# Performance work log

Measured on AMD Instinct MI355X. Metric: run time of the kernel, lower is better.

The kernel has to match this reference:

```python
import jax, jax.numpy as jnp
import numpy as np

D = 1024      # d_model
H = 16        # n_heads
KVH = 4       # num_kv_heads
DH = D // H   # head_dim = 64
CHUNK = 256
SDIM = 128
MG = 8        # m_global
B, T = 4, 4096


def setup_inputs() -> dict:
    key = jax.random.key(0)
    ks = jax.random.split(key, 12)
    s = 0.02
    mk = lambda i, shape: jax.random.normal(ks[i], shape, jnp.float32) * s
    return dict(
        x=jax.random.normal(ks[0], (B, T, D), jnp.float32),
        state=jnp.zeros((B, SDIM), jnp.float32),
        Wq=mk(1, (D, D)), Wk=mk(2, (KVH * DH, D)), Wv=mk(3, (KVH * DH, D)),
        Wo=mk(4, (D, D)), bo=jnp.zeros((D,), jnp.float32),
        ln_attn_g=jnp.ones((D,), jnp.float32), ln_attn_b=jnp.zeros((D,), jnp.float32),
        ln_ffn_g=jnp.ones((D,), jnp.float32), ln_ffn_b=jnp.zeros((D,), jnp.float32),
        W1=mk(5, (4 * D, D)), b1=jnp.zeros((4 * D,), jnp.float32),
        W2=mk(6, (D, 4 * D)), b2=jnp.zeros((D,), jnp.float32),
        Wsp=mk(7, (SDIM, D)), bsp=jnp.zeros((SDIM,), jnp.float32),
        Wsi=mk(8, (D, SDIM)), bsi=jnp.zeros((D,), jnp.float32),
        gtok=mk(9, (MG, D)),
    )


def _ln(x, g, b):
    m = x.mean(-1, keepdims=True)
    v = ((x - m) ** 2).mean(-1, keepdims=True)
    return (x - m) / jnp.sqrt(v + 1e-5) * g + b


def reference(x, state, Wq, Wk, Wv, Wo, bo, ln_attn_g, ln_attn_b,
              ln_ffn_g, ln_ffn_b, W1, b1, W2, b2, Wsp, bsp, Wsi, bsi, gtok):
    Bn, Tn, Dn = x.shape
    nchunks = Tn // CHUNK
    Tc = MG + CHUNK            # tokens per attention call (globals + chunk)
    G = H // KVH               # query heads per KV head
    causal = jnp.tril(jnp.ones((Tc, Tc), bool))
    scale = 1.0 / np.sqrt(DH).astype(np.float32)

    def step(st, chunk):  # st:[B,SDIM], chunk:[B,CHUNK,D]
        h = _ln(chunk, ln_attn_g, ln_attn_b) + (st @ Wsi.T + bsi)[:, None, :]
        h_in = jnp.concatenate([jnp.broadcast_to(gtok, (Bn, MG, Dn)), h], axis=1)
        q = (h_in @ Wq.T).reshape(Bn, Tc, H, DH)
        k = (h_in @ Wk.T).reshape(Bn, Tc, KVH, DH)
        v = (h_in @ Wv.T).reshape(Bn, Tc, KVH, DH)
        # GQA: group query heads over shared KV heads
        qg = q.reshape(Bn, Tc, KVH, G, DH)
        scores = jnp.einsum('bqhgd,bkhd->bhgqk', qg * scale, k)
        scores = jnp.where(causal, scores, -jnp.inf)
        attn = jax.nn.softmax(scores, axis=-1)
        o = jnp.einsum('bhgqk,bkhd->bqhgd', attn, v).reshape(Bn, Tc, Dn)
        y = (o @ Wo.T + bo)[:, MG:, :]
        c = chunk + y
        ff = jax.nn.gelu(_ln(c, ln_ffn_g, ln_ffn_b) @ W1.T + b1, approximate=False) @ W2.T + b2
        c = c + ff
        new_st = c.mean(axis=1) @ Wsp.T + bsp
        return new_st, c

    chunks = x.reshape(Bn, nchunks, CHUNK, Dn).transpose(1, 0, 2, 3)
    final_state, outs = jax.lax.scan(step, state, chunks)
    y_full = outs.transpose(1, 0, 2, 3).reshape(Bn, Tn, Dn)
    return y_full, final_state
```

## Files before the change

kernel.cpp:

```cpp
#include <hip/hip_runtime.h>
#include <hip/hip_bf16.h>

#define Dm    1024
#define Hn    16
#define KVH   4
#define DH    64
#define CHUNK 256
#define SDIM  128
#define MG    8
#define Bn    4
#define Tn    4096
#define TC    264
#define NSTEP 16
#define TD    4194304L

typedef __attribute__((ext_vector_type(8))) short short8;
typedef __attribute__((ext_vector_type(4))) float floatx4;
typedef __hip_bfloat16 bf16;

__device__ __forceinline__ void gl16(const void* g, void* l) {
    using GP = const __attribute__((address_space(1))) char*;
    using LP = __attribute__((address_space(3))) char*;
    __builtin_amdgcn_global_load_lds((GP)g, (LP)l, 16, 0, 0);
}
__device__ __forceinline__ float b2f(short s) {
    unsigned int u = ((unsigned int)(unsigned short)s) << 16;
    float f; __builtin_memcpy(&f, &u, 4); return f;
}
__device__ __forceinline__ short f2b(float f) {
    bf16 h = __float2bfloat16(f);
    short s; __builtin_memcpy(&s, &h, 2); return s;
}


__global__ __launch_bounds__(512) void vcopy_k(const float* __restrict__ s, float* __restrict__ d, int n) {
    int i = blockIdx.x * 512 + threadIdx.x;
    if (i < n) d[i] = s[i];
}

__global__ __launch_bounds__(256) void cvt_bf16_k(const float* __restrict__ s, bf16* __restrict__ d, int n4) {
    int i = blockIdx.x * 256 + threadIdx.x;
    if (i >= n4) return;
    float4 v = ((const float4*)s)[i];
    bf16* o = d + i * 4;
    o[0] = __float2bfloat16(v.x); o[1] = __float2bfloat16(v.y);
    o[2] = __float2bfloat16(v.z); o[3] = __float2bfloat16(v.w);
}

__global__ __launch_bounds__(256) void wsiT_k(const float* __restrict__ Wsi, bf16* __restrict__ WsiT) {
    int idx = blockIdx.x * 256 + threadIdx.x;
    int s = idx >> 10, d = idx & 1023;
    WsiT[idx] = __float2bfloat16(Wsi[d * SDIM + s]);
}

__global__ __launch_bounds__(64) void bfused_k(const bf16* __restrict__ wqkv, const float* __restrict__ bsi,
                                               float* __restrict__ bfused) {
    int n = blockIdx.x * 64 + threadIdx.x;
    const bf16* wr = wqkv + (long)n * 1024;
    float a = 0.f;
    for (int k8 = 0; k8 < 128; ++k8) {
        short8 wv = *(const short8*)(wr + k8 * 8);
#pragma unroll
        for (int e = 0; e < 8; ++e) a += b2f(wv[e]) * bsi[k8 * 8 + e];
    }
    bfused[n] = a;
}

__global__ __launch_bounds__(64) void sib_k(const float* __restrict__ st, const bf16* __restrict__ Wf,
                                            const float* __restrict__ bfused, float* __restrict__ sib) {
    int b = blockIdx.x, n = blockIdx.y * 64 + threadIdx.x;
    const float* sr = st + b * SDIM;
    const bf16* wr = Wf + (long)n * SDIM;
    float a = bfused[n];
#pragma unroll
    for (int k8 = 0; k8 < 16; ++k8) {
        short8 wv = *(const short8*)(wr + k8 * 8);
#pragma unroll
        for (int e = 0; e < 8; ++e) a += sr[k8 * 8 + e] * b2f(wv[e]);
    }
    sib[b * 1536 + n] = a;
}

__global__ __launch_bounds__(192) void addsi_k(bf16* __restrict__ qkv_s, const float* __restrict__ sib) {
    int b = blockIdx.x, r = MG + blockIdx.y, n0 = threadIdx.x * 8;
    bf16* p = qkv_s + ((long)(b * TC + r) * 1536 + n0);
    const float* sb = sib + b * 1536 + n0;
    short8 v = *(const short8*)p;
    short8 o;
#pragma unroll
    for (int e = 0; e < 8; ++e) o[e] = f2b(b2f(v[e]) + sb[e]);
    *(short8*)p = o;
}

__global__ __launch_bounds__(256) void lng_k(const float* __restrict__ x, const float* __restrict__ gtok,
                                             const float* __restrict__ g, const float* __restrict__ be,
                                             bf16* __restrict__ lnxg, int gstep) {
    int bx = blockIdx.x, b = blockIdx.y, tid = threadIdx.x;
    int sl = bx / 264, r = bx - sl * 264;
    bf16* orow = lnxg + (long)((sl * 4 + b) * 264 + r) * 1024 + tid * 4;
    if (r < MG) {
        float4 v = *(const float4*)(gtok + r * 1024 + tid * 4);
        orow[0] = __float2bfloat16(v.x); orow[1] = __float2bfloat16(v.y);
        orow[2] = __float2bfloat16(v.z); orow[3] = __float2bfloat16(v.w);
        return;
    }
    const float* row = x + (long)b * TD + ((long)(gstep * 4 + sl) * 256 + (r - MG)) * 1024;
    float4 v = *(const float4*)(row + tid * 4);
    float s = v.x + v.y + v.z + v.w;
    float q = v.x * v.x + v.y * v.y + v.z * v.z + v.w * v.w;
    for (int off = 32; off > 0; off >>= 1) { s += __shfl_down(s, off); q += __shfl_down(q, off); }
    __shared__ float red[10];
    int w = tid >> 6;
    if ((tid & 63) == 0) { red[w] = s; red[4 + w] = q; }
    __syncthreads();
    if (tid == 0) {
        float ts = red[0] + red[1] + red[2] + red[3];
        float tq = red[4] + red[5] + red[6] + red[7];
        float mean = ts * (1.f / Dm);
        float var = tq * (1.f / Dm) - mean * mean;
        red[8] = mean;
        red[9] = rsqrtf(var + 1e-5f);
    }
    __syncthreads();
    float mean = red[8], rstd = red[9];
    int d = tid * 4;
    float4 gv = *(const float4*)(g + d);
    float4 bv = *(const float4*)(be + d);
    orow[0] = __float2bfloat16((v.x - mean) * rstd * gv.x + bv.x);
    orow[1] = __float2bfloat16((v.y - mean) * rstd * gv.y + bv.y);
    orow[2] = __float2bfloat16((v.z - mean) * rstd * gv.z + bv.z);
    orow[3] = __float2bfloat16((v.w - mean) * rstd * gv.w + bv.w);
}

template<int BN>
__global__ __launch_bounds__(256) void gemm64(
    const bf16* __restrict__ A, const bf16* __restrict__ W,
    int M, int N, int K, int kspan,
    bf16* __restrict__ Cb, int ldc, const float* __restrict__ bias, int gelu,
    float* __restrict__ Cpart, long partMN)
{
    constexpr int NSEG = 4 + BN / 16;
    constexpr int SEGW = NSEG / 4;
    constexpr int FC   = BN / 64;
    constexpr int WN   = BN / 4;
    constexpr int HALFB = NSEG * 1024;
    constexpr int PHB   = 2 * HALFB;
    __shared__ short S[PHB];

    int tid = threadIdx.x;
    int w = tid >> 6, l = tid & 63;
    int m0 = blockIdx.y << 6, n0 = blockIdx.x * BN;
    long kb = (long)blockIdx.z * kspan;

    const bf16* gp[SEGW];
    int so[SEGW];
#pragma unroll
    for (int si = 0; si < SEGW; ++si) {
        int s = w + si * 4;
        const bf16* base = (s < 4) ? (A + (long)(m0 + s * 16 + (l >> 2)) * K)
                                   : (W + (long)(n0 + (s - 4) * 16 + (l >> 2)) * K);
        gp[si] = base + ((l & 3) << 3) + kb;
        so[si] = s * 1024 + l * 16;
    }
    char* cS = (char*)S;

    floatx4 acc[4][FC];
#pragma unroll
    for (int t = 0; t < 4; ++t)
#pragma unroll
        for (int u = 0; u < FC; ++u) acc[t][u] = (floatx4){0.f, 0.f, 0.f, 0.f};

    int arow = l & 15;
    int acol = (l >> 4) << 3;
    int np = kspan >> 6;

#define STAGE(p)                                                         \
    {                                                                    \
        int kt_ = (p) << 6;                                              \
        char* b_ = cS + ((p) & 1) * PHB;                                 \
        _Pragma("unroll")                                                \
        for (int si = 0; si < SEGW; ++si) {                              \
            gl16(gp[si] + kt_, b_ + so[si]);                             \
            gl16(gp[si] + kt_ + 32, b_ + HALFB + so[si]);                \
        }                                                                \
    }

    STAGE(0)
    for (int p = 0; p < np; ++p) {
        if (p + 1 < np) {
            STAGE(p + 1)
            if constexpr (SEGW == 2) asm volatile("s_waitcnt vmcnt(4)" ::: "memory");
            else                     asm volatile("s_waitcnt vmcnt(6)" ::: "memory");
        } else {
            asm volatile("s_waitcnt vmcnt(0)" ::: "memory");
        }
        __builtin_amdgcn_s_barrier();
        __builtin_amdgcn_sched_barrier(0);
        const short* buf = S + (p & 1) * (PHB / 2);
#pragma unroll
        for (int kh = 0; kh < 2; ++kh) {
            const short* hb = buf + kh * (HALFB / 2);
            short8 a[4], b[FC];
#pragma unroll
            for (int t = 0; t < 4; ++t)
                a[t] = *(const short8*)&hb[(t * 16 + arow) * 32 + acol];
#pragma unroll
            for (int u = 0; u < FC; ++u)
                b[u] = *(const short8*)&hb[2048 + (w * WN + u * 16 + arow) * 32 + acol];
#pragma unroll
            for (int t = 0; t < 4; ++t)
#pragma unroll
                for (int u = 0; u < FC; ++u)
                    acc[t][u] = __builtin_amdgcn_mfma_f32_16x16x32_bf16(a[t], b[u], acc[t][u], 0, 0, 0);
        }
        __builtin_amdgcn_sched_barrier(0);
        __builtin_amdgcn_s_barrier();
    }
#undef STAGE

    int crow0 = m0 + ((l >> 4) << 2);
    int ccol0 = n0 + w * WN + (l & 15);
    if (Cpart) {
        float* pp = Cpart + (long)blockIdx.z * partMN;
#pragma unroll
        for (int t = 0; t < 4; ++t)
#pragma unroll
            for (int rr = 0; rr < 4; ++rr) {
                int m = crow0 + t * 16 + rr;
                if (m >= M) continue;
#pragma unroll
                for (int u = 0; u < FC; ++u)
                    pp[(long)m * N + ccol0 + u * 16] = acc[t][u][rr];
            }
    } else {
#pragma unroll
        for (int t = 0; t < 4; ++t)
#pragma unroll
            for (int rr = 0; rr < 4; ++rr) {
                int m = crow0 + t * 16 + rr;
                if (m >= M) continue;
                bf16* crow = Cb + (long)m * ldc;
#pragma unroll
                for (int u = 0; u < FC; ++u) {
                    int n = ccol0 + u * 16;
                    float v = acc[t][u][rr];
                    if (bias) v += bias[n];
                    if (gelu) v = 0.5f * v * (1.f + erff(v * 0.70710678118654752f));
                    crow[n] = __float2bfloat16(v);
                }
            }
    }
}

__global__ __launch_bounds__(256) void reduce_ln_k(const float* __restrict__ part,
                                                   const float* __restrict__ bo,
                                                   const float* __restrict__ x,
                                                   float* __restrict__ out, long roff,
                                                   const float* __restrict__ g,
                                                   const float* __restrict__ be,
                                                   bf16* __restrict__ t_ln) {
    int m = blockIdx.x;
    int b = m >> 8, r = m & 255;
    int tid = threadIdx.x;
    long ro = (long)b * TD + (roff + r) * 1024L + tid * 4;
    int pi = m * 256 + tid;
    float4 s  = ((const float4*)part)[pi];
    float4 p2 = ((const float4*)(part + 1048576))[pi];
    float4 bv = ((const float4*)bo)[tid];
    float4 rv = *(const float4*)(x + ro);
    float c0 = s.x + p2.x + bv.x + rv.x;
    float c1 = s.y + p2.y + bv.y + rv.y;
    float c2 = s.z + p2.z + bv.z + rv.z;
    float c3 = s.w + p2.w + bv.w + rv.w;
    *(float4*)(out + ro) = make_float4(c0, c1, c2, c3);
    float sum = c0 + c1 + c2 + c3;
    float sq  = c0 * c0 + c1 * c1 + c2 * c2 + c3 * c3;
    for (int off = 32; off > 0; off >>= 1) { sum += __shfl_down(sum, off); sq += __shfl_down(sq, off); }
    __shared__ float red[10];
    int w = tid >> 6;
    if ((tid & 63) == 0) { red[w] = sum; red[4 + w] = sq; }
    __syncthreads();
    if (tid == 0) {
        float ts = red[0] + red[1] + red[2] + red[3];
        float tq = red[4] + red[5] + red[6] + red[7];
        float mean = ts * (1.f / Dm);
        float var = tq * (1.f / Dm) - mean * mean;
        red[8] = mean;
        red[9] = rsqrtf(var + 1e-5f);
    }
    __syncthreads();
    float mean = red[8], rstd = red[9];
    float4 gv = ((const float4*)g)[tid];
    float4 bev = ((const float4*)be)[tid];
    bf16* orow = t_ln + (long)(b * CHUNK + r) * Dm + tid * 4;
    orow[0] = __float2bfloat16((c0 - mean) * rstd * gv.x + bev.x);
    orow[1] = __float2bfloat16((c1 - mean) * rstd * gv.y + bev.y);
    orow[2] = __float2bfloat16((c2 - mean) * rstd * gv.z + bev.z);
    orow[3] = __float2bfloat16((c3 - mean) * rstd * gv.w + bev.w);
}

__global__ __launch_bounds__(256) void reduce_colpart_k(const float* __restrict__ part,
                                                        const float* __restrict__ bias,
                                                        float* __restrict__ out, long roff,
                                                        float* __restrict__ colp) {
    int b = blockIdx.x, rg = blockIdx.y, tid = threadIdx.x;
    float4 bv = ((const float4*)bias)[tid];
    float4 cs = make_float4(0.f, 0.f, 0.f, 0.f);
#pragma unroll
    for (int r8 = 0; r8 < 8; ++r8) {
        int r = rg * 8 + r8;
        int pi = (b * 256 + r) * 256 + tid;
        float4 s  = ((const float4*)part)[pi];
        float4 p2 = ((const float4*)(part + 1048576))[pi];
        long ro = (long)b * TD + (roff + r) * 1024L + tid * 4;
        float4 rv = *(const float4*)(out + ro);
        float4 v = make_float4(s.x + p2.x + bv.x + rv.x, s.y + p2.y + bv.y + rv.y,
                               s.z + p2.z + bv.z + rv.z, s.w + p2.w + bv.w + rv.w);
        *(float4*)(out + ro) = v;
        cs.x += v.x; cs.y += v.y; cs.z += v.z; cs.w += v.w;
    }
    *(float4*)(colp + ((b * 32 + rg) << 10) + tid * 4) = cs;
}

__global__ __launch_bounds__(256) void attn_mfma_k(const bf16* __restrict__ qkv, bf16* __restrict__ o_mat) {
    int qc = blockIdx.x, head = blockIdx.y, b = blockIdx.z;
    int kvh = head >> 2;
    int tid = threadIdx.x, w = tid >> 6, l = tid & 63;
    int m16 = l & 15, h4 = l >> 4;

    __shared__ short Qs[64][64];
    __shared__ short Ks[64][64];
    __shared__ short Vt[64][64];
    __shared__ short Ps[4][16][64];

    const long rowq0 = (long)b * TC + MG + qc * 64;
    const bf16* kbase = qkv + ((long)b * TC) * 1536 + 1024 + kvh * DH;
    const bf16* vbase = kbase + 256;

#pragma unroll
    for (int p = 0; p < 2; ++p) {
        int rr = p * 32 + (tid >> 3);
        gl16(qkv + (rowq0 + rr) * 1536 + head * DH + (tid & 7) * 8, &Qs[rr][(tid & 7) * 8]);
    }

    float a_m[4] = {-1e30f, -1e30f, -1e30f, -1e30f};
    float a_l[4] = {0.f, 0.f, 0.f, 0.f};
    floatx4 acc_o[4];
#pragma unroll
    for (int dt = 0; dt < 4; ++dt) acc_o[dt] = (floatx4){0.f, 0.f, 0.f, 0.f};
    short8 aq[2];

    int qtok0 = MG + qc * 64 + w * 16 + h4 * 4;
    int ntiles = qc + 2;

    for (int t = 0; t < ntiles; ++t) {
        int jt = t * 64;
#pragma unroll
        for (int p = 0; p < 2; ++p) {
            int rr = p * 32 + (tid >> 3);
            int gk = min(jt + rr, TC - 1);
            gl16(kbase + (long)gk * 1536 + (tid & 7) * 8, &Ks[rr][(tid & 7) * 8]);
        }
#pragma unroll
        for (int p = 0; p < 2; ++p) {
            int cg = p * 4 + w;
            int gk = min(jt + l, TC - 1);
            short8 vv = *(const short8*)(vbase + (long)gk * 1536 + cg * 8);
#pragma unroll
            for (int e = 0; e < 8; ++e) Vt[cg * 8 + e][l] = vv[e];
        }
        __syncthreads();
        if (t == 0) {
            aq[0] = *(const short8*)&Qs[w * 16 + m16][h4 * 8];
            aq[1] = *(const short8*)&Qs[w * 16 + m16][32 + h4 * 8];
        }
        floatx4 s[4];
#pragma unroll
        for (int st = 0; st < 4; ++st) {
            s[st] = (floatx4){0.f, 0.f, 0.f, 0.f};
#pragma unroll
            for (int c = 0; c < 2; ++c) {
                short8 kf = *(const short8*)&Ks[st * 16 + m16][c * 32 + h4 * 8];
                s[st] = __builtin_amdgcn_mfma_f32_16x16x32_bf16(aq[c], kf, s[st], 0, 0, 0);
            }
        }
#pragma unroll
        for (int st = 0; st < 4; ++st) {
            int keyg = jt + st * 16 + m16;
#pragma unroll
            for (int r = 0; r < 4; ++r) {
                float v = s[st][r] * 0.125f;
                s[st][r] = (keyg > qtok0 + r) ? -1e30f : v;
            }
        }
#pragma unroll
        for (int r = 0; r < 4; ++r) {
            float tm = fmaxf(fmaxf(s[0][r], s[1][r]), fmaxf(s[2][r], s[3][r]));
            tm = fmaxf(tm, __shfl_xor(tm, 1));
            tm = fmaxf(tm, __shfl_xor(tm, 2));
            tm = fmaxf(tm, __shfl_xor(tm, 4));
            tm = fmaxf(tm, __shfl_xor(tm, 8));
            float mn = fmaxf(a_m[r], tm);
            float rs = __expf(a_m[r] - mn);
            a_m[r] = mn;
            float ps = 0.f;
#pragma unroll
            for (int st = 0; st < 4; ++st) {
                float p = __expf(s[st][r] - mn);
                s[st][r] = p;
                ps += p;
            }
            ps += __shfl_xor(ps, 1); ps += __shfl_xor(ps, 2);
            ps += __shfl_xor(ps, 4); ps += __shfl_xor(ps, 8);
            a_l[r] = a_l[r] * rs + ps;
#pragma unroll
            for (int dt = 0; dt < 4; ++dt) acc_o[dt][r] *= rs;
#pragma unroll
            for (int st = 0; st < 4; ++st) {
                Ps[w][h4 * 4 + r][st * 16 + m16] = f2b(s[st][r]);
            }
        }
#pragma unroll
        for (int c = 0; c < 2; ++c) {
            short8 ap = *(const short8*)&Ps[w][m16][c * 32 + h4 * 8];
#pragma unroll
            for (int dt = 0; dt < 4; ++dt) {
                short8 vf = *(const short8*)&Vt[dt * 16 + m16][c * 32 + h4 * 8];
                acc_o[dt] = __builtin_amdgcn_mfma_f32_16x16x32_bf16(ap, vf, acc_o[dt], 0, 0, 0);
            }
        }
        __syncthreads();
    }

#pragma unroll
    for (int r = 0; r < 4; ++r) {
        float inv = 1.f / a_l[r];
        long row = (long)b * CHUNK + qc * 64 + w * 16 + h4 * 4 + r;
#pragma unroll
        for (int dt = 0; dt < 4; ++dt)
            o_mat[row * Dm + head * DH + dt * 16 + m16] = __float2bfloat16(acc_o[dt][r] * inv);
    }
}

__global__ __launch_bounds__(256) void state_update_k(const float* __restrict__ colp,
                                                      const float* __restrict__ Wsp,
                                                      const float* __restrict__ bsp,
                                                      float* __restrict__ st) {
    int b = blockIdx.x;
    int tid = threadIdx.x, w = tid >> 6, l = tid & 63;
    int ss = blockIdx.y * 4 + w;
    float4 m[4];
#pragma unroll
    for (int t = 0; t < 4; ++t) m[t] = make_float4(0.f, 0.f, 0.f, 0.f);
    for (int rg = 0; rg < 32; ++rg) {
        const float* pr = colp + ((b * 32 + rg) << 10) + l * 16;
#pragma unroll
        for (int t = 0; t < 4; ++t) {
            float4 v = *(const float4*)(pr + t * 4);
            m[t].x += v.x; m[t].y += v.y; m[t].z += v.z; m[t].w += v.w;
        }
    }
    const float* wr = Wsp + (long)ss * Dm + l * 16;
    float a = 0.f;
#pragma unroll
    for (int t = 0; t < 4; ++t) {
        float4 wv = *(const float4*)(wr + t * 4);
        a += m[t].x * wv.x + m[t].y * wv.y + m[t].z * wv.z + m[t].w * wv.w;
    }
    a *= (1.f / CHUNK);
    for (int off = 32; off > 0; off >>= 1) a += __shfl_down(a, off);
    if (l == 0) st[b * SDIM + ss] = a + bsp[ss];
}


extern "C" void kernel_launch(void* const* d_in, const int* in_sizes, int n_in,
                              void* d_out, int out_size, void* d_ws, size_t ws_size,
                              hipStream_t stream) {
    const float* x     = (const float*)d_in[0];
    const float* state = (const float*)d_in[1];
    const float* Wq    = (const float*)d_in[2];
    const float* Wk    = (const float*)d_in[3];
    const float* Wv    = (const float*)d_in[4];
    const float* Wo    = (const float*)d_in[5];
    const float* bo    = (const float*)d_in[6];
    const float* lag   = (const float*)d_in[7];
    const float* lab   = (const float*)d_in[8];
    const float* lfg   = (const float*)d_in[9];
    const float* lfb   = (const float*)d_in[10];
    const float* W1    = (const float*)d_in[11];
    const float* b1    = (const float*)d_in[12];
    const float* W2    = (const float*)d_in[13];
    const float* b2    = (const float*)d_in[14];
    const float* Wsp   = (const float*)d_in[15];
    const float* bsp   = (const float*)d_in[16];
    const float* Wsi   = (const float*)d_in[17];
    const float* bsi   = (const float*)d_in[18];
    const float* gtok  = (const float*)d_in[19];

    float* out = (float*)d_out;
    char*  wsb = (char*)d_ws;

    bf16* wqkv   = (bf16*)(wsb);
    bf16* wo     = (bf16*)(wsb + 3145728);
    bf16* w1     = (bf16*)(wsb + 5242880);
    bf16* w2     = (bf16*)(wsb + 13631488);
    bf16* Wfused = (bf16*)(wsb + 22020096);
    bf16* WsiT   = (bf16*)(wsb + 22413312);
    float* bfused= (float*)(wsb + 22675456);
    float* sib   = (float*)(wsb + 22681600);
    float* st    = (float*)(wsb + 22706176);
    bf16* qkvg   = (bf16*)(wsb + 22708224);
    char* R1     = wsb + 35684352;
    bf16* lnxg   = (bf16*)R1;
    bf16* u      = (bf16*)R1;
    float* part  = (float*)(wsb + 44335104);
    char* scrB   = wsb + 52723712;
    bf16* o_mat  = (bf16*)scrB;
    bf16* t_ln   = (bf16*)scrB;
    float* colp  = (float*)scrB;

    vcopy_k<<<1, 512, 0, stream>>>(state, st, 512);
    cvt_bf16_k<<<1024, 256, 0, stream>>>(Wq, wqkv,            262144);
    cvt_bf16_k<<< 256, 256, 0, stream>>>(Wk, wqkv + 1048576,   65536);
    cvt_bf16_k<<< 256, 256, 0, stream>>>(Wv, wqkv + 1310720,   65536);
    cvt_bf16_k<<<1024, 256, 0, stream>>>(Wo, wo,              262144);
    cvt_bf16_k<<<4096, 256, 0, stream>>>(W1, w1,             1048576);
    cvt_bf16_k<<<4096, 256, 0, stream>>>(W2, w2,             1048576);
    wsiT_k<<<512, 256, 0, stream>>>(Wsi, WsiT);
    gemm64<64><<<dim3(2, 24, 1), 256, 0, stream>>>(
        wqkv, WsiT, 1536, 128, 1024, 1024,
        Wfused, 128, nullptr, 0, nullptr, 0L);
    bfused_k<<<24, 64, 0, stream>>>(wqkv, bsi, bfused);

    for (int s = 0; s < NSTEP; ++s) {
        long roff = (long)s * CHUNK;
        if ((s & 3) == 0) {
            int g = s >> 2;
            lng_k<<<dim3(1056, 4), 256, 0, stream>>>(x, gtok, lag, lab, lnxg, g);
            gemm64<64><<<dim3(24, 66, 1), 256, 0, stream>>>(
                lnxg, wqkv, 4224, 1536, 1024, 1024,
                qkvg, 1536, nullptr, 0, nullptr, 0L);
        }
        bf16* qkv_s = qkvg + (long)(s & 3) * (4 * 264 * 1536);
        sib_k<<<dim3(4, 24), 64, 0, stream>>>(st, Wfused, bfused, sib);
        addsi_k<<<dim3(4, 256), 192, 0, stream>>>(qkv_s, sib);
        attn_mfma_k<<<dim3(4, 16, 4), 256, 0, stream>>>(qkv_s, o_mat);
        gemm64<64><<<dim3(16, 16, 2), 256, 0, stream>>>(
            o_mat, wo, Bn * CHUNK, 1024, 1024, 512,
            nullptr, 0, nullptr, 0, part, 1048576L);
        reduce_ln_k<<<1024, 256, 0, stream>>>(part, bo, x, out, roff, lfg, lfb, t_ln);
        gemm64<128><<<dim3(32, 16, 1), 256, 0, stream>>>(
            t_ln, w1, Bn * CHUNK, 4096, 1024, 1024,
            u, 4096, b1, 1, nullptr, 0L);
        gemm64<64><<<dim3(16, 16, 2), 256, 0, stream>>>(
            u, w2, Bn * CHUNK, 1024, 4096, 2048,
            nullptr, 0, nullptr, 0, part, 1048576L);
        reduce_colpart_k<<<dim3(4, 32), 256, 0, stream>>>(part, b2, out, roff, colp);
        state_update_k<<<dim3(4, 32), 256, 0, stream>>>(colp, Wsp, bsp, st);
    }
    vcopy_k<<<1, 512, 0, stream>>>(st, out + (long)Bn * Tn * Dm, 512);
}
```

Baseline: 1.580 ms.

## Fuse state-injection bias into attention loads and merge state update with sib

Result: slower. 1.914 ms (+21.1%).

```diff
diff --git a/kernel.cpp b/kernel.cpp
--- a/kernel.cpp
+++ b/kernel.cpp
@@ -79,17 +79,6 @@
         for (int e = 0; e < 8; ++e) a += sr[k8 * 8 + e] * b2f(wv[e]);
     }
     sib[b * 1536 + n] = a;
-}
-
-__global__ __launch_bounds__(192) void addsi_k(bf16* __restrict__ qkv_s, const float* __restrict__ sib) {
-    int b = blockIdx.x, r = MG + blockIdx.y, n0 = threadIdx.x * 8;
-    bf16* p = qkv_s + ((long)(b * TC + r) * 1536 + n0);
-    const float* sb = sib + b * 1536 + n0;
-    short8 v = *(const short8*)p;
-    short8 o;
-#pragma unroll
-    for (int e = 0; e < 8; ++e) o[e] = f2b(b2f(v[e]) + sb[e]);
-    *(short8*)p = o;
 }
 
 __global__ __launch_bounds__(256) void lng_k(const float* __restrict__ x, const float* __restrict__ gtok,
@@ -322,7 +311,49 @@
     *(float4*)(colp + ((b * 32 + rg) << 10) + tid * 4) = cs;
 }
 
-__global__ __launch_bounds__(256) void attn_mfma_k(const bf16* __restrict__ qkv, bf16* __restrict__ o_mat) {
+__global__ __launch_bounds__(1024) void state_sib_k(const float* __restrict__ colp,
+                                                    const float* __restrict__ Wsp,
+                                                    const float* __restrict__ bsp,
+                                                    const bf16* __restrict__ Wf,
+                                                    const float* __restrict__ bfused,
+                                                    float* __restrict__ st,
+                                                    float* __restrict__ sib) {
+    int b = blockIdx.x, tid = threadIdx.x;
+    __shared__ float cm[1024];
+    __shared__ float sts[128];
+    float s = 0.f;
+#pragma unroll
+    for (int rg = 0; rg < 32; ++rg) s += colp[((b * 32 + rg) << 10) + tid];
+    cm[tid] = s * (1.f / CHUNK);
+    __syncthreads();
+    int w = tid >> 6, l = tid & 63;
+#pragma unroll
+    for (int i = 0; i < 8; ++i) {
+        int ss = w * 8 + i;
+        const float* wr = Wsp + (long)ss * Dm + l * 16;
+        float a = 0.f;
+#pragma unroll
+        for (int t = 0; t < 16; ++t) a += wr[t] * cm[l * 16 + t];
+        for (int off = 32; off > 0; off >>= 1) a += __shfl_down(a, off);
+        if (l == 0) { float v = a + bsp[ss]; sts[ss] = v; st[b * SDIM + ss] = v; }
+    }
+    __syncthreads();
+    for (int n = tid; n < 1536; n += 1024) {
+        const bf16* wr = Wf + (long)n * SDIM;
+        float a = bfused[n];
+#pragma unroll
+        for (int k8 = 0; k8 < 16; ++k8) {
+            short8 wv = *(const short8*)(wr + k8 * 8);
+#pragma unroll
+            for (int e = 0; e < 8; ++e) a += sts[k8 * 8 + e] * b2f(wv[e]);
+        }
+        sib[b * 1536 + n] = a;
+    }
+}
+
+__global__ __launch_bounds__(256) void attn_mfma_k(const bf16* __restrict__ qkv,
+                                                   const float* __restrict__ sib,
+                                                   bf16* __restrict__ o_mat) {
     int qc = blockIdx.x, head = blockIdx.y, b = blockIdx.z;
     int kvh = head >> 2;
     int tid = threadIdx.x, w = tid >> 6, l = tid & 63;
@@ -332,15 +363,26 @@
     __shared__ short Ks[64][64];
     __shared__ short Vt[64][64];
     __shared__ short Ps[4][16][64];
+    __shared__ float sq[64], sk[64], sv[64];
 
     const long rowq0 = (long)b * TC + MG + qc * 64;
     const bf16* kbase = qkv + ((long)b * TC) * 1536 + 1024 + kvh * DH;
     const bf16* vbase = kbase + 256;
 
+    if (tid < 64)       sq[tid]       = sib[b * 1536 + head * 64 + tid];
+    else if (tid < 128) sk[tid - 64]  = sib[b * 1536 + 1024 + kvh * 64 + (tid - 64)];
+    else if (tid < 192) sv[tid - 128] = sib[b * 1536 + 1280 + kvh * 64 + (tid - 128)];
+    __syncthreads();
+
 #pragma unroll
     for (int p = 0; p < 2; ++p) {
         int rr = p * 32 + (tid >> 3);
-        gl16(qkv + (rowq0 + rr) * 1536 + head * DH + (tid & 7) * 8, &Qs[rr][(tid & 7) * 8]);
+        int c0 = (tid & 7) * 8;
+        short8 v = *(const short8*)(qkv + (rowq0 + rr) * 1536 + head * DH + c0);
+        short8 o;
+#pragma unroll
+        for (int e = 0; e < 8; ++e) o[e] = f2b(b2f(v[e]) + sq[c0 + e]);
+        *(short8*)&Qs[rr][c0] = o;
     }
 
     float a_m[4] = {-1e30f, -1e30f, -1e30f, -1e30f};
@@ -358,14 +400,25 @@
 #pragma unroll
         for (int p = 0; p < 2; ++p) {
             int rr = p * 32 + (tid >> 3);
+            int c0 = (tid & 7) * 8;
             int gk = min(jt + rr, TC - 1);
-            gl16(kbase + (long)gk * 1536 + (tid & 7) * 8, &Ks[rr][(tid & 7) * 8]);
+            short8 v = *(const short8*)(kbase + (long)gk * 1536 + c0);
+            short8 o;
+            if (gk >= MG) {
+#pragma unroll
+                for (int e = 0; e < 8; ++e) o[e] = f2b(b2f(v[e]) + sk[c0 + e]);
+            } else o = v;
+            *(short8*)&Ks[rr][c0] = o;
         }
 #pragma unroll
         for (int p = 0; p < 2; ++p) {
             int cg = p * 4 + w;
             int gk = min(jt + l, TC - 1);
             short8 vv = *(const short8*)(vbase + (long)gk * 1536 + cg * 8);
+            if (gk >= MG) {
+#pragma unroll
+                for (int e = 0; e < 8; ++e) vv[e] = f2b(b2f(vv[e]) + sv[cg * 8 + e]);
+            }
 #pragma unroll
             for (int e = 0; e < 8; ++e) Vt[cg * 8 + e][l] = vv[e];
         }
@@ -440,36 +493,6 @@
         for (int dt = 0; dt < 4; ++dt)
             o_mat[row * Dm + head * DH + dt * 16 + m16] = __float2bfloat16(acc_o[dt][r] * inv);
     }
-}
-
-__global__ __launch_bounds__(256) void state_update_k(const float* __restrict__ colp,
-                                                      const float* __restrict__ Wsp,
-                                                      const float* __restrict__ bsp,
-                                                      float* __restrict__ st) {
-    int b = blockIdx.x;
-    int tid = threadIdx.x, w = tid >> 6, l = tid & 63;
-    int ss = blockIdx.y * 4 + w;
-    float4 m[4];
-#pragma unroll
-    for (int t = 0; t < 4; ++t) m[t] = make_float4(0.f, 0.f, 0.f, 0.f);
-    for (int rg = 0; rg < 32; ++rg) {
-        const float* pr = colp + ((b * 32 + rg) << 10) + l * 16;
-#pragma unroll
-        for (int t = 0; t < 4; ++t) {
-            float4 v = *(const float4*)(pr + t * 4);
-            m[t].x += v.x; m[t].y += v.y; m[t].z += v.z; m[t].w += v.w;
-        }
-    }
-    const float* wr = Wsp + (long)ss * Dm + l * 16;
-    float a = 0.f;
-#pragma unroll
-    for (int t = 0; t < 4; ++t) {
-        float4 wv = *(const float4*)(wr + t * 4);
-        a += m[t].x * wv.x + m[t].y * wv.y + m[t].z * wv.z + m[t].w * wv.w;
-    }
-    a *= (1.f / CHUNK);
-    for (int off = 32; off > 0; off >>= 1) a += __shfl_down(a, off);
-    if (l == 0) st[b * SDIM + ss] = a + bsp[ss];
 }
 
 
@@ -531,20 +554,19 @@
         wqkv, WsiT, 1536, 128, 1024, 1024,
         Wfused, 128, nullptr, 0, nullptr, 0L);
     bfused_k<<<24, 64, 0, stream>>>(wqkv, bsi, bfused);
+    sib_k<<<dim3(4, 24), 64, 0, stream>>>(st, Wfused, bfused, sib);
 
     for (int s = 0; s < NSTEP; ++s) {
         long roff = (long)s * CHUNK;
         if ((s & 3) == 0) {
             int g = s >> 2;
             lng_k<<<dim3(1056, 4), 256, 0, stream>>>(x, gtok, lag, lab, lnxg, g);
-            gemm64<64><<<dim3(24, 66, 1), 256, 0, stream>>>(
+            gemm64<128><<<dim3(12, 66, 1), 256, 0, stream>>>(
                 lnxg, wqkv, 4224, 1536, 1024, 1024,
                 qkvg, 1536, nullptr, 0, nullptr, 0L);
         }
-        bf16* qkv_s = qkvg + (long)(s & 3) * (4 * 264 * 1536);
-        sib_k<<<dim3(4, 24), 64, 0, stream>>>(st, Wfused, bfused, sib);
-        addsi_k<<<dim3(4, 256), 192, 0, stream>>>(qkv_s, sib);
-        attn_mfma_k<<<dim3(4, 16, 4), 256, 0, stream>>>(qkv_s, o_mat);
+        const bf16* qkv_s = qkvg + (long)(s & 3) * (4 * 264 * 1536);
+        attn_mfma_k<<<dim3(4, 16, 4), 256, 0, stream>>>(qkv_s, sib, o_mat);
         gemm64<64><<<dim3(16, 16, 2), 256, 0, stream>>>(
             o_mat, wo, Bn * CHUNK, 1024, 1024, 512,
             nullptr, 0, nullptr, 0, part, 1048576L);
@@ -556,7 +578,7 @@
             u, w2, Bn * CHUNK, 1024, 4096, 2048,
             nullptr, 0, nullptr, 0, part, 1048576L);
         reduce_colpart_k<<<dim3(4, 32), 256, 0, stream>>>(part, b2, out, roff, colp);
-        state_update_k<<<dim3(4, 32), 256, 0, stream>>>(colp, Wsp, bsp, st);
+        state_sib_k<<<4, 1024, 0, stream>>>(colp, Wsp, bsp, Wfused, bfused, st, sib);
     }
     vcopy_k<<<1, 512, 0, stream>>>(st, out + (long)Bn * Tn * Dm, 512);
 }
```

## Fuse state-injection bias into attention kernel and widen QKV GEMM tile

Applied to the files above, without the earlier changes.

Result: faster. 1.540 ms (-2.6%).

```diff
diff --git a/kernel.cpp b/kernel.cpp
--- a/kernel.cpp
+++ b/kernel.cpp
@@ -64,32 +64,6 @@
         for (int e = 0; e < 8; ++e) a += b2f(wv[e]) * bsi[k8 * 8 + e];
     }
     bfused[n] = a;
-}
-
-__global__ __launch_bounds__(64) void sib_k(const float* __restrict__ st, const bf16* __restrict__ Wf,
-                                            const float* __restrict__ bfused, float* __restrict__ sib) {
-    int b = blockIdx.x, n = blockIdx.y * 64 + threadIdx.x;
-    const float* sr = st + b * SDIM;
-    const bf16* wr = Wf + (long)n * SDIM;
-    float a = bfused[n];
-#pragma unroll
-    for (int k8 = 0; k8 < 16; ++k8) {
-        short8 wv = *(const short8*)(wr + k8 * 8);
-#pragma unroll
-        for (int e = 0; e < 8; ++e) a += sr[k8 * 8 + e] * b2f(wv[e]);
-    }
-    sib[b * 1536 + n] = a;
-}
-
-__global__ __launch_bounds__(192) void addsi_k(bf16* __restrict__ qkv_s, const float* __restrict__ sib) {
-    int b = blockIdx.x, r = MG + blockIdx.y, n0 = threadIdx.x * 8;
-    bf16* p = qkv_s + ((long)(b * TC + r) * 1536 + n0);
-    const float* sb = sib + b * 1536 + n0;
-    short8 v = *(const short8*)p;
-    short8 o;
-#pragma unroll
-    for (int e = 0; e < 8; ++e) o[e] = f2b(b2f(v[e]) + sb[e]);
-    *(short8*)p = o;
 }
 
 __global__ __launch_bounds__(256) void lng_k(const float* __restrict__ x, const float* __restrict__ gtok,
@@ -322,7 +296,41 @@
     *(float4*)(colp + ((b * 32 + rg) << 10) + tid * 4) = cs;
 }
 
-__global__ __launch_bounds__(256) void attn_mfma_k(const bf16* __restrict__ qkv, bf16* __restrict__ o_mat) {
+__global__ __launch_bounds__(256) void state_update_k(const float* __restrict__ colp,
+                                                      const float* __restrict__ Wsp,
+                                                      const float* __restrict__ bsp,
+                                                      float* __restrict__ st) {
+    int b = blockIdx.x;
+    int tid = threadIdx.x, w = tid >> 6, l = tid & 63;
+    int ss = blockIdx.y * 4 + w;
+    float4 m[4];
+#pragma unroll
+    for (int t = 0; t < 4; ++t) m[t] = make_float4(0.f, 0.f, 0.f, 0.f);
+    for (int rg = 0; rg < 32; ++rg) {
+        const float* pr = colp + ((b * 32 + rg) << 10) + l * 16;
+#pragma unroll
+        for (int t = 0; t < 4; ++t) {
+            float4 v = *(const float4*)(pr + t * 4);
+            m[t].x += v.x; m[t].y += v.y; m[t].z += v.z; m[t].w += v.w;
+        }
+    }
+    const float* wr = Wsp + (long)ss * Dm + l * 16;
+    float a = 0.f;
+#pragma unroll
+    for (int t = 0; t < 4; ++t) {
+        float4 wv = *(const float4*)(wr + t * 4);
+        a += m[t].x * wv.x + m[t].y * wv.y + m[t].z * wv.z + m[t].w * wv.w;
+    }
+    a *= (1.f / CHUNK);
+    for (int off = 32; off > 0; off >>= 1) a += __shfl_down(a, off);
+    if (l == 0) st[b * SDIM + ss] = a + bsp[ss];
+}
+
+__global__ __launch_bounds__(256) void attn_mfma_k(const bf16* __restrict__ qkv,
+                                                   const float* __restrict__ st,
+                                                   const bf16* __restrict__ Wf,
+                                                   const float* __restrict__ bfused,
+                                                   bf16* __restrict__ o_mat) {
     int qc = blockIdx.x, head = blockIdx.y, b = blockIdx.z;
     int kvh = head >> 2;
     int tid = threadIdx.x, w = tid >> 6, l = tid & 63;
@@ -332,15 +340,39 @@
     __shared__ short Ks[64][64];
     __shared__ short Vt[64][64];
     __shared__ short Ps[4][16][64];
+    __shared__ float sq[64], sk[64], sv[64];
 
     const long rowq0 = (long)b * TC + MG + qc * 64;
     const bf16* kbase = qkv + ((long)b * TC) * 1536 + 1024 + kvh * DH;
     const bf16* vbase = kbase + 256;
 
+    if (tid < 192) {
+        int which = tid >> 6, nn = tid & 63;
+        int n = (which == 0) ? head * 64 + nn
+              : (which == 1) ? 1024 + kvh * 64 + nn
+                             : 1280 + kvh * 64 + nn;
+        const bf16* wr = Wf + (long)n * SDIM;
+        const float* sr = st + b * SDIM;
+        float a = bfused[n];
+#pragma unroll
+        for (int k8 = 0; k8 < 16; ++k8) {
+            short8 wv = *(const short8*)(wr + k8 * 8);
+#pragma unroll
+            for (int e = 0; e < 8; ++e) a += sr[k8 * 8 + e] * b2f(wv[e]);
+        }
+        if (which == 0) sq[nn] = a; else if (which == 1) sk[nn] = a; else sv[nn] = a;
+    }
+    __syncthreads();
+
 #pragma unroll
     for (int p = 0; p < 2; ++p) {
         int rr = p * 32 + (tid >> 3);
-        gl16(qkv + (rowq0 + rr) * 1536 + head * DH + (tid & 7) * 8, &Qs[rr][(tid & 7) * 8]);
+        int c0 = (tid & 7) * 8;
+        short8 v = *(const short8*)(qkv + (rowq0 + rr) * 1536 + head * DH + c0);
+        short8 o;
+#pragma unroll
+        for (int e = 0; e < 8; ++e) o[e] = f2b(b2f(v[e]) + sq[c0 + e]);
+        *(short8*)&Qs[rr][c0] = o;
     }
 
     float a_m[4] = {-1e30f, -1e30f, -1e30f, -1e30f};
@@ -358,14 +390,25 @@
 #pragma unroll
         for (int p = 0; p < 2; ++p) {
             int rr = p * 32 + (tid >> 3);
+            int c0 = (tid & 7) * 8;
             int gk = min(jt + rr, TC - 1);
-            gl16(kbase + (long)gk * 1536 + (tid & 7) * 8, &Ks[rr][(tid & 7) * 8]);
+            short8 v = *(const short8*)(kbase + (long)gk * 1536 + c0);
+            short8 o;
+            if (gk >= MG) {
+#pragma unroll
+                for (int e = 0; e < 8; ++e) o[e] = f2b(b2f(v[e]) + sk[c0 + e]);
+            } else o = v;
+            *(short8*)&Ks[rr][c0] = o;
         }
 #pragma unroll
         for (int p = 0; p < 2; ++p) {
             int cg = p * 4 + w;
             int gk = min(jt + l, TC - 1);
             short8 vv = *(const short8*)(vbase + (long)gk * 1536 + cg * 8);
+            if (gk >= MG) {
+#pragma unroll
+                for (int e = 0; e < 8; ++e) vv[e] = f2b(b2f(vv[e]) + sv[cg * 8 + e]);
+            }
 #pragma unroll
             for (int e = 0; e < 8; ++e) Vt[cg * 8 + e][l] = vv[e];
         }
@@ -376,21 +419,21 @@
         }
         floatx4 s[4];
 #pragma unroll
-        for (int st = 0; st < 4; ++st) {
-            s[st] = (floatx4){0.f, 0.f, 0.f, 0.f};
+        for (int st_ = 0; st_ < 4; ++st_) {
+            s[st_] = (floatx4){0.f, 0.f, 0.f, 0.f};
 #pragma unroll
             for (int c = 0; c < 2; ++c) {
-                short8 kf = *(const short8*)&Ks[st * 16 + m16][c * 32 + h4 * 8];
-                s[st] = __builtin_amdgcn_mfma_f32_16x16x32_bf16(aq[c], kf, s[st], 0, 0, 0);
-            }
-        }
-#pragma unroll
-        for (int st = 0; st < 4; ++st) {
-            int keyg = jt + st * 16 + m16;
+                short8 kf = *(const short8*)&Ks[st_ * 16 + m16][c * 32 + h4 * 8];
+                s[st_] = __builtin_amdgcn_mfma_f32_16x16x32_bf16(aq[c], kf, s[st_], 0, 0, 0);
+            }
+        }
+#pragma unroll
+        for (int st_ = 0; st_ < 4; ++st_) {
+            int keyg = jt + st_ * 16 + m16;
 #pragma unroll
             for (int r = 0; r < 4; ++r) {
-                float v = s[st][r] * 0.125f;
-                s[st][r] = (keyg > qtok0 + r) ? -1e30f : v;
+                float v = s[st_][r] * 0.125f;
+                s[st_][r] = (keyg > qtok0 + r) ? -1e30f : v;
             }
         }
 #pragma unroll
@@ -405,9 +448,9 @@
             a_m[r] = mn;
             float ps = 0.f;
 #pragma unroll
-            for (int st = 0; st < 4; ++st) {
-                float p = __expf(s[st][r] - mn);
-                s[st][r] = p;
+            for (int st_ = 0; st_ < 4; ++st_) {
+                float p = __expf(s[st_][r] - mn);
+                s[st_][r] = p;
                 ps += p;
             }
             ps += __shfl_xor(ps, 1); ps += __shfl_xor(ps, 2);
@@ -416,8 +459,8 @@
 #pragma unroll
             for (int dt = 0; dt < 4; ++dt) acc_o[dt][r] *= rs;
 #pragma unroll
-            for (int st = 0; st < 4; ++st) {
-                Ps[w][h4 * 4 + r][st * 16 + m16] = f2b(s[st][r]);
+            for (int st_ = 0; st_ < 4; ++st_) {
+                Ps[w][h4 * 4 + r][st_ * 16 + m16] = f2b(s[st_][r]);
             }
         }
 #pragma unroll
@@ -440,36 +483,6 @@
         for (int dt = 0; dt < 4; ++dt)
             o_mat[row * Dm + head * DH + dt * 16 + m16] = __float2bfloat16(acc_o[dt][r] * inv);
     }
-}
-
-__global__ __launch_bounds__(256) void state_update_k(const float* __restrict__ colp,
-                                                      const float* __restrict__ Wsp,
-                                                      const float* __restrict__ bsp,
-                                                      float* __restrict__ st) {
-    int b = blockIdx.x;
-    int tid = threadIdx.x, w = tid >> 6, l = tid & 63;
-    int ss = blockIdx.y * 4 + w;
-    float4 m[4];
-#pragma unroll
-    for (int t = 0; t < 4; ++t) m[t] = make_float4(0.f, 0.f, 0.f, 0.f);
-    for (int rg = 0; rg < 32; ++rg) {
-        const float* pr = colp + ((b * 32 + rg) << 10) + l * 16;
-#pragma unroll
-        for (int t = 0; t < 4; ++t) {
-            float4 v = *(const float4*)(pr + t * 4);
-            m[t].x += v.x; m[t].y += v.y; m[t].z += v.z; m[t].w += v.w;
-        }
-    }
-    const float* wr = Wsp + (long)ss * Dm + l * 16;
-    float a = 0.f;
-#pragma unroll
-    for (int t = 0; t < 4; ++t) {
-        float4 wv = *(const float4*)(wr + t * 4);
-        a += m[t].x * wv.x + m[t].y * wv.y + m[t].z * wv.z + m[t].w * wv.w;
-    }
-    a *= (1.f / CHUNK);
-    for (int off = 32; off > 0; off >>= 1) a += __shfl_down(a, off);
-    if (l == 0) st[b * SDIM + ss] = a + bsp[ss];
 }
 
 
@@ -507,7 +520,6 @@
     bf16* Wfused = (bf16*)(wsb + 22020096);
     bf16* WsiT   = (bf16*)(wsb + 22413312);
     float* bfused= (float*)(wsb + 22675456);
-    float* sib   = (float*)(wsb + 22681600);
     float* st    = (float*)(wsb + 22706176);
     bf16* qkvg   = (bf16*)(wsb + 22708224);
     char* R1     = wsb + 35684352;
@@ -537,14 +549,12 @@
         if ((s & 3) == 0) {
             int g = s >> 2;
             lng_k<<<dim3(1056, 4), 256, 0, stream>>>(x, gtok, lag, lab, lnxg, g);
-            gemm64<64><<<dim3(24, 66, 1), 256, 0, stream>>>(
+            gemm64<128><<<dim3(12, 66, 1), 256, 0, stream>>>(
                 lnxg, wqkv, 4224, 1536, 1024, 1024,
                 qkvg, 1536, nullptr, 0, nullptr, 0L);
         }
-        bf16* qkv_s = qkvg + (long)(s & 3) * (4 * 264 * 1536);
-        sib_k<<<dim3(4, 24), 64, 0, stream>>>(st, Wfused, bfused, sib);
-        addsi_k<<<dim3(4, 256), 192, 0, stream>>>(qkv_s, sib);
-        attn_mfma_k<<<dim3(4, 16, 4), 256, 0, stream>>>(qkv_s, o_mat);
+        const bf16* qkv_s = qkvg + (long)(s & 3) * (4 * 264 * 1536);
+        attn_mfma_k<<<dim3(4, 16, 4), 256, 0, stream>>>(qkv_s, st, Wfused, bfused, o_mat);
         gemm64<64><<<dim3(16, 16, 2), 256, 0, stream>>>(
             o_mat, wo, Bn * CHUNK, 1024, 1024, 512,
             nullptr, 0, nullptr, 0, part, 1048576L);
```
